# Kernel tuning notes

Measured on AMD Instinct MI355X. Metric: run time of the kernel, lower is better.

Reference implementation:

```python
import jax, jax.numpy as jnp
import numpy as np

N_NODES = 2_000_000
HIDDEN = 128
NUM_SEGMENTS = 8192


def setup_inputs() -> dict:
    key = jax.random.key(0)
    kx, kw, ks = jax.random.split(key, 3)
    x = jax.random.normal(kx, (N_NODES, HIDDEN), dtype=jnp.float32)
    w = jax.random.normal(kw, (HIDDEN, 1), dtype=jnp.float32)
    segment_ids = jnp.sort(jax.random.randint(ks, (N_NODES,), 0, NUM_SEGMENTS, dtype=jnp.int32))
    return {"x": x, "w": w, "segment_ids": segment_ids}


def reference(x, w, segment_ids):
    # scores: per-node scalar from Linear(hidden, 1, bias=False)
    s = (x @ w)[:, 0]  # [N]
    # segment softmax over each subgraph (dim=0 within a segment)
    smax = jax.ops.segment_max(s, segment_ids, num_segments=NUM_SEGMENTS,
                               indices_are_sorted=True)  # [G]
    e = jnp.exp(s - smax[segment_ids])  # [N]
    denom = jax.ops.segment_sum(e, segment_ids, num_segments=NUM_SEGMENTS,
                                indices_are_sorted=True)  # [G]
    denom = jnp.where(denom == 0, 1.0, denom)  # guard empty segments
    p = e / denom[segment_ids]  # [N]
    # weighted sum pooling per subgraph -> [G, hidden]
    pooled = jax.ops.segment_sum(x * p[:, None], segment_ids,
                                 num_segments=NUM_SEGMENTS,
                                 indices_are_sorted=True)
    return pooled
```

## Files before the change

### kernel.cpp

```cpp
#include <hip/hip_runtime.h>
#include <math.h>

#define HIDDEN 128

__global__ void seg_bounds_kernel(const int* __restrict__ seg,
                                  int* __restrict__ offs,
                                  int n, int num_seg) {
    int i = blockIdx.x * blockDim.x + threadIdx.x;
    if (i > n) return;
    int cur  = (i < n) ? seg[i]     : num_seg;
    int prev = (i > 0) ? seg[i - 1] : -1;
    for (int g = prev + 1; g <= cur; ++g) offs[g] = i;
}

__global__ __launch_bounds__(256, 8)
void attn_pool_kernel(const float* __restrict__ x,
                      const float* __restrict__ w,
                      const int* __restrict__ offs,
                      float* __restrict__ out,
                      int num_seg) {
    const int g = blockIdx.x * 4 + (threadIdx.x >> 6);
    if (g >= num_seg) return;
    const int lane = threadIdx.x & 63;
    const int half = lane >> 5;
    const int sub  = lane & 31;

    const float4 wv = *reinterpret_cast<const float4*>(w + (sub << 2));

    const int start = offs[g];
    const int end   = offs[g + 1];

    if (end <= start) {
        if (half == 0) {
            *reinterpret_cast<float4*>(out + (size_t)g * HIDDEN + (sub << 2)) =
                make_float4(0.f, 0.f, 0.f, 0.f);
        }
        return;
    }

    float  m    = -INFINITY;
    float  dsum = 0.f;
    float4 acc  = make_float4(0.f, 0.f, 0.f, 0.f);

    for (int r = start + half; r < end; r += 2) {
        const float4 v = *reinterpret_cast<const float4*>(
            x + (size_t)r * HIDDEN + (sub << 2));
        float p = v.x * wv.x + v.y * wv.y + v.z * wv.z + v.w * wv.w;
        p += __shfl_xor(p, 1);
        p += __shfl_xor(p, 2);
        p += __shfl_xor(p, 4);
        p += __shfl_xor(p, 8);
        p += __shfl_xor(p, 16);
        const float mn = fmaxf(m, p);
        const float sc = __expf(m - mn);
        const float e  = __expf(p - mn);
        dsum  = dsum  * sc + e;
        acc.x = acc.x * sc + v.x * e;
        acc.y = acc.y * sc + v.y * e;
        acc.z = acc.z * sc + v.z * e;
        acc.w = acc.w * sc + v.w * e;
        m = mn;
    }

    const float m1 = __shfl_xor(m, 32);
    const float d1 = __shfl_xor(dsum, 32);
    float4 a1;
    a1.x = __shfl_xor(acc.x, 32);
    a1.y = __shfl_xor(acc.y, 32);
    a1.z = __shfl_xor(acc.z, 32);
    a1.w = __shfl_xor(acc.w, 32);

    const float mf = fmaxf(m, m1);
    const float s0 = __expf(m - mf);
    const float s1 = __expf(m1 - mf);
    const float df = dsum * s0 + d1 * s1;
    const float inv = 1.0f / df;

    if (half == 0) {
        float4 o;
        o.x = (acc.x * s0 + a1.x * s1) * inv;
        o.y = (acc.y * s0 + a1.y * s1) * inv;
        o.z = (acc.z * s0 + a1.z * s1) * inv;
        o.w = (acc.w * s0 + a1.w * s1) * inv;
        *reinterpret_cast<float4*>(out + (size_t)g * HIDDEN + (sub << 2)) = o;
    }
}

extern "C" void kernel_launch(void* const* d_in, const int* in_sizes, int n_in,
                              void* d_out, int out_size, void* d_ws, size_t ws_size,
                              hipStream_t stream) {
    const float* x   = (const float*)d_in[0];
    const float* w   = (const float*)d_in[1];
    const int*   seg = (const int*)d_in[2];
    float*       out = (float*)d_out;

    const int n       = in_sizes[2];
    const int num_seg = out_size / HIDDEN;
    int* offs = (int*)d_ws;

    {
        const int threads = 256;
        const int blocks  = (n + 1 + threads - 1) / threads;
        seg_bounds_kernel<<<blocks, threads, 0, stream>>>(seg, offs, n, num_seg);
    }
    {
        const int blocks = (num_seg + 3) / 4;
        attn_pool_kernel<<<blocks, 256, 0, stream>>>(x, w, offs, out, num_seg);
    }
}
```

Measured before the change: 1.281 ms.

## Process four rows per wave with 8-float lanes and register prefetch of next row

Each wave now splits into four 16-lane groups, each handling a different row with two float4 loads per lane, instead of two 32-lane halves. The next row's data is loaded into registers before the current row is processed, so more memory requests are in flight to hide latency. Partial softmax states are merged across groups with a two-step shuffle reduction. The cost is more registers per thread, and the launch bound drops from 8 to 4 waves, which reduces occupancy.

```diff
diff --git a/kernel.cpp b/kernel.cpp
--- a/kernel.cpp
+++ b/kernel.cpp
@@ -2,6 +2,7 @@
 #include <math.h>
 
 #define HIDDEN 128
+#define NEG_BIG (-3.0e38f)
 
 __global__ void seg_bounds_kernel(const int* __restrict__ seg,
                                   int* __restrict__ offs,
@@ -13,7 +14,7 @@
     for (int g = prev + 1; g <= cur; ++g) offs[g] = i;
 }
 
-__global__ __launch_bounds__(256, 8)
+__global__ __launch_bounds__(256, 4)
 void attn_pool_kernel(const float* __restrict__ x,
                       const float* __restrict__ w,
                       const int* __restrict__ offs,
@@ -22,67 +23,118 @@
     const int g = blockIdx.x * 4 + (threadIdx.x >> 6);
     if (g >= num_seg) return;
     const int lane = threadIdx.x & 63;
-    const int half = lane >> 5;
-    const int sub  = lane & 31;
+    const int grp  = lane >> 4;
+    const int sub  = lane & 15;
 
-    const float4 wv = *reinterpret_cast<const float4*>(w + (sub << 2));
+    const float4 wa = *reinterpret_cast<const float4*>(w + sub * 8);
+    const float4 wb = *reinterpret_cast<const float4*>(w + sub * 8 + 4);
 
     const int start = offs[g];
     const int end   = offs[g + 1];
 
     if (end <= start) {
-        if (half == 0) {
-            *reinterpret_cast<float4*>(out + (size_t)g * HIDDEN + (sub << 2)) =
-                make_float4(0.f, 0.f, 0.f, 0.f);
+        if (lane < 16) {
+            const float4 z = make_float4(0.f, 0.f, 0.f, 0.f);
+            float* o = out + (size_t)g * HIDDEN + sub * 8;
+            *reinterpret_cast<float4*>(o)     = z;
+            *reinterpret_cast<float4*>(o + 4) = z;
         }
         return;
     }
 
-    float  m    = -INFINITY;
-    float  dsum = 0.f;
-    float4 acc  = make_float4(0.f, 0.f, 0.f, 0.f);
+    float  m = NEG_BIG, dsum = 0.f;
+    float4 acca = make_float4(0.f, 0.f, 0.f, 0.f);
+    float4 accb = make_float4(0.f, 0.f, 0.f, 0.f);
 
-    for (int r = start + half; r < end; r += 2) {
-        const float4 v = *reinterpret_cast<const float4*>(
-            x + (size_t)r * HIDDEN + (sub << 2));
-        float p = v.x * wv.x + v.y * wv.y + v.z * wv.z + v.w * wv.w;
-        p += __shfl_xor(p, 1);
-        p += __shfl_xor(p, 2);
-        p += __shfl_xor(p, 4);
-        p += __shfl_xor(p, 8);
-        p += __shfl_xor(p, 16);
-        const float mn = fmaxf(m, p);
-        const float sc = __expf(m - mn);
-        const float e  = __expf(p - mn);
-        dsum  = dsum  * sc + e;
-        acc.x = acc.x * sc + v.x * e;
-        acc.y = acc.y * sc + v.y * e;
-        acc.z = acc.z * sc + v.z * e;
-        acc.w = acc.w * sc + v.w * e;
-        m = mn;
+    const int cnt = end - start;
+    const int L   = (cnt + 3) >> 2;
+
+    int row  = start + grp;
+    {
+        int rowc = min(row, end - 1);
+        const float* p0 = x + (size_t)rowc * HIDDEN + sub * 8;
+        float4 a = reinterpret_cast<const float4*>(p0)[0];
+        float4 b = reinterpret_cast<const float4*>(p0)[1];
+
+        for (int i = 0; i < L; ++i) {
+            const int rown = row + 4;
+            float4 an = make_float4(0.f, 0.f, 0.f, 0.f);
+            float4 bn = make_float4(0.f, 0.f, 0.f, 0.f);
+            if (i + 1 < L) {
+                const int rowcn = min(rown, end - 1);
+                const float* pn = x + (size_t)rowcn * HIDDEN + sub * 8;
+                an = reinterpret_cast<const float4*>(pn)[0];
+                bn = reinterpret_cast<const float4*>(pn)[1];
+            }
+
+            float p = a.x * wa.x + a.y * wa.y + a.z * wa.z + a.w * wa.w
+                    + b.x * wb.x + b.y * wb.y + b.z * wb.z + b.w * wb.w;
+            p += __shfl_xor(p, 1);
+            p += __shfl_xor(p, 2);
+            p += __shfl_xor(p, 4);
+            p += __shfl_xor(p, 8);
+
+            const bool act = (row < end);
+            p = act ? p : NEG_BIG;
+
+            const float mn = fmaxf(m, p);
+            const float sc = __expf(m - mn);
+            const float e  = act ? __expf(p - mn) : 0.f;
+
+            dsum   = dsum   * sc + e;
+            acca.x = acca.x * sc + a.x * e;
+            acca.y = acca.y * sc + a.y * e;
+            acca.z = acca.z * sc + a.z * e;
+            acca.w = acca.w * sc + a.w * e;
+            accb.x = accb.x * sc + b.x * e;
+            accb.y = accb.y * sc + b.y * e;
+            accb.z = accb.z * sc + b.z * e;
+            accb.w = accb.w * sc + b.w * e;
+            m = mn;
+
+            a = an; b = bn; row = rown;
+        }
     }
 
-    const float m1 = __shfl_xor(m, 32);
-    const float d1 = __shfl_xor(dsum, 32);
-    float4 a1;
-    a1.x = __shfl_xor(acc.x, 32);
-    a1.y = __shfl_xor(acc.y, 32);
-    a1.z = __shfl_xor(acc.z, 32);
-    a1.w = __shfl_xor(acc.w, 32);
+    #pragma unroll
+    for (int mask = 16; mask <= 32; mask <<= 1) {
+        const float mo = __shfl_xor(m, mask);
+        const float d1 = __shfl_xor(dsum, mask);
+        float4 ao, bo;
+        ao.x = __shfl_xor(acca.x, mask);
+        ao.y = __shfl_xor(acca.y, mask);
+        ao.z = __shfl_xor(acca.z, mask);
+        ao.w = __shfl_xor(acca.w, mask);
+        bo.x = __shfl_xor(accb.x, mask);
+        bo.y = __shfl_xor(accb.y, mask);
+        bo.z = __shfl_xor(accb.z, mask);
+        bo.w = __shfl_xor(accb.w, mask);
 
-    const float mf = fmaxf(m, m1);
-    const float s0 = __expf(m - mf);
-    const float s1 = __expf(m1 - mf);
-    const float df = dsum * s0 + d1 * s1;
-    const float inv = 1.0f / df;
+        const float mf = fmaxf(m, mo);
+        const float s0 = __expf(m  - mf);
+        const float s1 = __expf(mo - mf);
+        dsum   = dsum * s0 + d1 * s1;
+        acca.x = acca.x * s0 + ao.x * s1;
+        acca.y = acca.y * s0 + ao.y * s1;
+        acca.z = acca.z * s0 + ao.z * s1;
+        acca.w = acca.w * s0 + ao.w * s1;
+        accb.x = accb.x * s0 + bo.x * s1;
+        accb.y = accb.y * s0 + bo.y * s1;
+        accb.z = accb.z * s0 + bo.z * s1;
+        accb.w = accb.w * s0 + bo.w * s1;
+        m = mf;
+    }
 
-    if (half == 0) {
-        float4 o;
-        o.x = (acc.x * s0 + a1.x * s1) * inv;
-        o.y = (acc.y * s0 + a1.y * s1) * inv;
-        o.z = (acc.z * s0 + a1.z * s1) * inv;
-        o.w = (acc.w * s0 + a1.w * s1) * inv;
-        *reinterpret_cast<float4*>(out + (size_t)g * HIDDEN + (sub << 2)) = o;
+    if (lane < 16) {
+        const float inv = 1.0f / dsum;
+        float4 oa, ob;
+        oa.x = acca.x * inv; oa.y = acca.y * inv;
+        oa.z = acca.z * inv; oa.w = acca.w * inv;
+        ob.x = accb.x * inv; ob.y = accb.y * inv;
+        ob.z = accb.z * inv; ob.w = accb.w * inv;
+        float* o = out + (size_t)g * HIDDEN + sub * 8;
+        *reinterpret_cast<float4*>(o)     = oa;
+        *reinterpret_cast<float4*>(o + 4) = ob;
     }
 }
 
```

Result: no change. 1.277 ms (-0.3%).
